# Optimization experiments

Hardware: AMD Instinct MI355X
Metric: run time of the kernel (lower is better)

## Reference

```python
import jax, jax.numpy as jnp
import numpy as np

B, P, C = 2, 2048, 64
SIZE = 128          # image_size
K = 8               # points_per_pixel (z-buffer depth)
RADIUS = 1.5        # in pixels
RAD_POW = 2
TAU = 1.0
BIG = 1e10          # sentinel z for pixels a point does not cover


def setup_inputs() -> dict:
    key = jax.random.key(0)
    k1, k2, k3 = jax.random.split(key, 3)
    xy = jax.random.uniform(k1, (B, P, 2), minval=-1.0, maxval=1.0)   # NDC xy
    z = jax.random.uniform(k2, (B, P, 1), minval=0.1, maxval=10.0)    # depth > 0
    pts3D = jnp.concatenate([xy, z], axis=-1)                          # [B,P,3]
    src = jax.random.normal(k3, (B, C, P), dtype=jnp.float32)          # [B,C,P]
    return {"pts3D": pts3D, "src": src}


def reference(pts3D, src):
    # --- sign flips from the torch forward: pts[:, :, :2] *= -1 ---
    pts = pts3D * jnp.array([-1.0, -1.0, 1.0], dtype=pts3D.dtype)
    px, py, pz = pts[..., 0], pts[..., 1], pts[..., 2]                 # [B,P]

    r_ndc = float(RADIUS) / float(SIZE) * 2.0

    # pixel-center NDC grid (pytorch3d convention: +x left, +y up)
    ii = jnp.arange(SIZE, dtype=pts.dtype)
    ndc = 1.0 - 2.0 * (ii + 0.5) / SIZE                                # [SIZE]

    # squared NDC distance pixel->point: [B,H,W,P]
    dx = ndc[None, None, :, None] - px[:, None, None, :]               # [B,1,W,P]
    dy = ndc[None, :, None, None] - py[:, None, None, :]               # [B,H,1,P]
    d2 = dx * dx + dy * dy                                             # [B,H,W,P]

    # rasterize_points: per pixel, K nearest-in-z points within radius
    inside = d2 <= r_ndc * r_ndc
    zkey = jnp.where(inside, pz[:, None, None, :], jnp.asarray(BIG, d2.dtype))
    neg_top, idx = jax.lax.top_k(-zkey, K)            # smallest z first, [B,H,W,K]
    valid = (-neg_top) < BIG                           # idx >= 0 equivalent

    dist = jnp.take_along_axis(d2, idx, axis=-1)       # [B,H,W,K]
    dist = dist / (r_ndc ** RAD_POW)

    # alphas = (1 - clamp(dist,0.001,1)^0.5)^tau
    alphas = (1.0 - jnp.sqrt(jnp.clip(dist, 0.001, 1.0))) ** TAU
    alphas = jnp.where(valid, alphas, 0.0)

    # alpha_composite: w_k = a_k * prod_{j<k} (1 - a_j), front-to-back
    T = jnp.cumprod(1.0 - alphas, axis=-1)
    w = alphas * jnp.concatenate([jnp.ones_like(T[..., :1]), T[..., :-1]], axis=-1)

    # gather features per batch: src [B,C,P], idx [B,H,W,K] -> [B,C,H,W,K]
    gathered = jax.vmap(lambda f, i: f[:, i])(src, idx)
    out = jnp.einsum('bchwk,bhwk->bchw', gathered, w)  # [B,C,H,W]
    return out
```

## Files before the change

### kernel.cpp

```cpp
#include <hip/hip_runtime.h>
#include <hip/hip_bf16.h>

#define BATCH 2
#define NPTS 2048
#define NCH 64
#define IMG 128
#define KTOP 8
#define BIGF 1e10f
#define CAP 128

__global__ __launch_bounds__(64) void raster_mega(
    const float* __restrict__ pts,
    const float* __restrict__ src,
    float* __restrict__ out) {
  __shared__ float4 cand[CAP];

  const int bid = blockIdx.x;
  const int cg = bid & 3;
  const int half = (bid >> 2) & 1;
  const int h = (bid >> 3) & 127;
  const int b = bid >> 10;
  const int lane = threadIdx.x;

  const float r_ndc = 0.0234375f;
  const float r2 = r_ndc * r_ndc;
  const float yc = 1.0f - 2.0f * (h + 0.5f) / 128.0f;

  const float* pb = pts + b * NPTS * 3;
  int base = 0;
  for (int it = 0; it < NPTS / 64; ++it) {
    int p = (it << 6) + lane;
    float y = pb[p * 3 + 1];
    float dy = yc + y;
    bool hit = (dy * dy <= r2);
    unsigned long long mask = __ballot(hit);
    if (mask) {
      if (hit) {
        int pos = base + __popcll(mask & ((1ull << lane) - 1ull));
        if (pos < CAP)
          cand[pos] = make_float4(pb[p * 3 + 0], y, pb[p * 3 + 2],
                                  __int_as_float(p));
      }
      base += __popcll(mask);
    }
  }
  __syncthreads();
  const int cnt = min(base, CAP);

  const int w = (half << 6) + lane;
  const float xc = 1.0f - 2.0f * (w + 0.5f) / 128.0f;

  float bz[KTOP], bd[KTOP];
  int bp[KTOP];
  #pragma unroll
  for (int k = 0; k < KTOP; ++k) { bz[k] = BIGF; bd[k] = 0.f; bp[k] = 0; }

  for (int j = 0; j < cnt; ++j) {
    float4 c4 = cand[j];
    float dx = xc + c4.x;
    float dyy = yc + c4.y;
    float d2 = dx * dx + dyy * dyy;
    if (d2 <= r2) {
      float cz = c4.z, cd = d2;
      int cp = __float_as_int(c4.w);
      #pragma unroll
      for (int s = 0; s < KTOP; ++s) {
        bool lt = (cz < bz[s]);
        float tz = bz[s], td = bd[s];
        int tp = bp[s];
        if (lt) { bz[s] = cz; bd[s] = cd; bp[s] = cp;
                  cz = tz; cd = td; cp = tp; }
      }
    }
  }

  float wgt[KTOP];
  float T = 1.0f;
  const float inv_r2 = 1.0f / r2;
  #pragma unroll
  for (int k = 0; k < KTOP; ++k) {
    float alpha = 0.0f;
    if (bz[k] < BIGF) {
      float dist = bd[k] * inv_r2;
      dist = fminf(fmaxf(dist, 0.001f), 1.0f);
      alpha = 1.0f - sqrtf(dist);
    }
    wgt[k] = alpha * T;
    T *= (1.0f - alpha);
  }

  const float* sb = src + ((size_t)b * NCH + cg * 16) * NPTS;
  float acc[16];
  #pragma unroll
  for (int c = 0; c < 16; ++c) acc[c] = 0.0f;
  #pragma unroll
  for (int k = 0; k < KTOP; ++k) {
    float wk = wgt[k];
    int p = bp[k];
    #pragma unroll
    for (int c = 0; c < 16; ++c)
      acc[c] += wk * sb[c * NPTS + p];
  }

  float* ob = out + (((size_t)b * NCH + cg * 16) * IMG + h) * IMG + w;
  const int S = IMG * IMG;
  #pragma unroll
  for (int c = 0; c < 16; ++c)
    ob[c * S] = acc[c];
}

extern "C" void kernel_launch(void* const* d_in, const int* in_sizes, int n_in,
                              void* d_out, int out_size, void* d_ws, size_t ws_size,
                              hipStream_t stream) {
  const float* pts = (const float*)d_in[0];
  const float* src = (const float*)d_in[1];
  float* out = (float*)d_out;

  raster_mega<<<BATCH * IMG * 2 * 4, 64, 0, stream>>>(pts, src, out);
}
```

Baseline: 83.73 us.

## Transpose src to point-major layout for vectorized feature gathers

```diff
diff --git a/kernel.cpp b/kernel.cpp
--- a/kernel.cpp
+++ b/kernel.cpp
@@ -1,5 +1,4 @@
 #include <hip/hip_runtime.h>
-#include <hip/hip_bf16.h>
 
 #define BATCH 2
 #define NPTS 2048
@@ -9,9 +8,31 @@
 #define BIGF 1e10f
 #define CAP 128
 
+__global__ __launch_bounds__(256) void transpose_src(
+    const float* __restrict__ src,
+    float* __restrict__ srcT) {
+  __shared__ float tile[64][65];
+  const int blk = blockIdx.x;
+  const int b = blk >> 5;
+  const int p0 = (blk & 31) << 6;
+  const int lane = threadIdx.x & 63;
+  const int wv = threadIdx.x >> 6;
+  #pragma unroll
+  for (int i = 0; i < 16; ++i) {
+    const int c = (i << 2) + wv;
+    tile[c][lane] = src[((size_t)b * NCH + c) * NPTS + p0 + lane];
+  }
+  __syncthreads();
+  #pragma unroll
+  for (int i = 0; i < 16; ++i) {
+    const int r = (i << 2) + wv;
+    srcT[((size_t)b * NPTS + p0 + r) * NCH + lane] = tile[lane][r];
+  }
+}
+
 __global__ __launch_bounds__(64) void raster_mega(
     const float* __restrict__ pts,
-    const float* __restrict__ src,
+    const float* __restrict__ srcT,
     float* __restrict__ out) {
   __shared__ float4 cand[CAP];
 
@@ -89,17 +110,25 @@
     T *= (1.0f - alpha);
   }
 
-  const float* sb = src + ((size_t)b * NCH + cg * 16) * NPTS;
+  const float* st = srcT + (size_t)b * NPTS * NCH + cg * 16;
   float acc[16];
   #pragma unroll
   for (int c = 0; c < 16; ++c) acc[c] = 0.0f;
   #pragma unroll
   for (int k = 0; k < KTOP; ++k) {
     float wk = wgt[k];
-    int p = bp[k];
-    #pragma unroll
-    for (int c = 0; c < 16; ++c)
-      acc[c] += wk * sb[c * NPTS + p];
+    if (wk != 0.0f) {
+      const float4* fp = (const float4*)(st + (size_t)bp[k] * NCH);
+      float4 f0 = fp[0], f1 = fp[1], f2 = fp[2], f3 = fp[3];
+      acc[0]  += wk * f0.x; acc[1]  += wk * f0.y;
+      acc[2]  += wk * f0.z; acc[3]  += wk * f0.w;
+      acc[4]  += wk * f1.x; acc[5]  += wk * f1.y;
+      acc[6]  += wk * f1.z; acc[7]  += wk * f1.w;
+      acc[8]  += wk * f2.x; acc[9]  += wk * f2.y;
+      acc[10] += wk * f2.z; acc[11] += wk * f2.w;
+      acc[12] += wk * f3.x; acc[13] += wk * f3.y;
+      acc[14] += wk * f3.z; acc[15] += wk * f3.w;
+    }
   }
 
   float* ob = out + (((size_t)b * NCH + cg * 16) * IMG + h) * IMG + w;
@@ -115,6 +144,8 @@
   const float* pts = (const float*)d_in[0];
   const float* src = (const float*)d_in[1];
   float* out = (float*)d_out;
+  float* srcT = (float*)d_ws;
 
-  raster_mega<<<BATCH * IMG * 2 * 4, 64, 0, stream>>>(pts, src, out);
+  transpose_src<<<BATCH * (NPTS / 64), 256, 0, stream>>>(src, srcT);
+  raster_mega<<<BATCH * IMG * 2 * 4, 64, 0, stream>>>(pts, srcT, out);
 }
```

Result: slower. 85.88 us (+2.6%).

## Share row candidate scan across four channel-group waves in one block

Applied to the files above, without the earlier changes.

```diff
diff --git a/kernel.cpp b/kernel.cpp
--- a/kernel.cpp
+++ b/kernel.cpp
@@ -1,5 +1,4 @@
 #include <hip/hip_runtime.h>
-#include <hip/hip_bf16.h>
 
 #define BATCH 2
 #define NPTS 2048
@@ -7,20 +6,23 @@
 #define IMG 128
 #define KTOP 8
 #define BIGF 1e10f
-#define CAP 128
+#define SEGCAP 128
+#define NSEG 4
 
-__global__ __launch_bounds__(64) void raster_mega(
+__global__ __launch_bounds__(256) void raster_mega(
     const float* __restrict__ pts,
     const float* __restrict__ src,
     float* __restrict__ out) {
-  __shared__ float4 cand[CAP];
+  __shared__ float4 cand[NSEG][SEGCAP];
+  __shared__ int scnt[NSEG];
 
   const int bid = blockIdx.x;
-  const int cg = bid & 3;
-  const int half = (bid >> 2) & 1;
-  const int h = (bid >> 3) & 127;
-  const int b = bid >> 10;
-  const int lane = threadIdx.x;
+  const int half = bid & 1;
+  const int h = (bid >> 1) & (IMG - 1);
+  const int b = bid >> 8;
+  const int t = threadIdx.x;
+  const int wv = t >> 6;
+  const int lane = t & 63;
 
   const float r_ndc = 0.0234375f;
   const float r2 = r_ndc * r_ndc;
@@ -28,8 +30,8 @@
 
   const float* pb = pts + b * NPTS * 3;
   int base = 0;
-  for (int it = 0; it < NPTS / 64; ++it) {
-    int p = (it << 6) + lane;
+  for (int it = 0; it < NPTS / (64 * NSEG); ++it) {
+    int p = (wv << 9) + (it << 6) + lane;
     float y = pb[p * 3 + 1];
     float dy = yc + y;
     bool hit = (dy * dy <= r2);
@@ -37,15 +39,15 @@
     if (mask) {
       if (hit) {
         int pos = base + __popcll(mask & ((1ull << lane) - 1ull));
-        if (pos < CAP)
-          cand[pos] = make_float4(pb[p * 3 + 0], y, pb[p * 3 + 2],
-                                  __int_as_float(p));
+        if (pos < SEGCAP)
+          cand[wv][pos] = make_float4(pb[p * 3 + 0], y, pb[p * 3 + 2],
+                                      __int_as_float(p));
       }
       base += __popcll(mask);
     }
   }
+  if (lane == 0) scnt[wv] = min(base, SEGCAP);
   __syncthreads();
-  const int cnt = min(base, CAP);
 
   const int w = (half << 6) + lane;
   const float xc = 1.0f - 2.0f * (w + 0.5f) / 128.0f;
@@ -55,21 +57,25 @@
   #pragma unroll
   for (int k = 0; k < KTOP; ++k) { bz[k] = BIGF; bd[k] = 0.f; bp[k] = 0; }
 
-  for (int j = 0; j < cnt; ++j) {
-    float4 c4 = cand[j];
-    float dx = xc + c4.x;
-    float dyy = yc + c4.y;
-    float d2 = dx * dx + dyy * dyy;
-    if (d2 <= r2) {
-      float cz = c4.z, cd = d2;
-      int cp = __float_as_int(c4.w);
-      #pragma unroll
-      for (int s = 0; s < KTOP; ++s) {
-        bool lt = (cz < bz[s]);
-        float tz = bz[s], td = bd[s];
-        int tp = bp[s];
-        if (lt) { bz[s] = cz; bd[s] = cd; bp[s] = cp;
-                  cz = tz; cd = td; cp = tp; }
+  #pragma unroll 1
+  for (int seg = 0; seg < NSEG; ++seg) {
+    const int cnt = scnt[seg];
+    for (int j = 0; j < cnt; ++j) {
+      float4 c4 = cand[seg][j];
+      float dx = xc + c4.x;
+      float dyy = yc + c4.y;
+      float d2 = dx * dx + dyy * dyy;
+      if (d2 <= r2) {
+        float cz = c4.z, cd = d2;
+        int cp = __float_as_int(c4.w);
+        #pragma unroll
+        for (int s = 0; s < KTOP; ++s) {
+          bool lt = (cz < bz[s]);
+          float tz = bz[s], td = bd[s];
+          int tp = bp[s];
+          if (lt) { bz[s] = cz; bd[s] = cd; bp[s] = cp;
+                    cz = tz; cd = td; cp = tp; }
+        }
       }
     }
   }
@@ -89,20 +95,22 @@
     T *= (1.0f - alpha);
   }
 
-  const float* sb = src + ((size_t)b * NCH + cg * 16) * NPTS;
+  const float* sb = src + ((size_t)b * NCH + wv * 16) * NPTS;
   float acc[16];
   #pragma unroll
   for (int c = 0; c < 16; ++c) acc[c] = 0.0f;
   #pragma unroll
   for (int k = 0; k < KTOP; ++k) {
     float wk = wgt[k];
-    int p = bp[k];
-    #pragma unroll
-    for (int c = 0; c < 16; ++c)
-      acc[c] += wk * sb[c * NPTS + p];
+    if (wk != 0.0f) {
+      int p = bp[k];
+      #pragma unroll
+      for (int c = 0; c < 16; ++c)
+        acc[c] += wk * sb[c * NPTS + p];
+    }
   }
 
-  float* ob = out + (((size_t)b * NCH + cg * 16) * IMG + h) * IMG + w;
+  float* ob = out + (((size_t)b * NCH + wv * 16) * IMG + h) * IMG + w;
   const int S = IMG * IMG;
   #pragma unroll
   for (int c = 0; c < 16; ++c)
@@ -116,5 +124,5 @@
   const float* src = (const float*)d_in[1];
   float* out = (float*)d_out;
 
-  raster_mega<<<BATCH * IMG * 2 * 4, 64, 0, stream>>>(pts, src, out);
+  raster_mega<<<BATCH * IMG * 2, 256, 0, stream>>>(pts, src, out);
 }
```

Result: faster. 78.13 us (-6.7%).
